# Performance work log

Hardware: AMD Instinct MI355X
Metric: run time of the kernel (lower is better)

Reference implementation:

```python
import jax, jax.numpy as jnp
import numpy as np

WH, WW = 7, 7
DIM, HEADS = 256, 8


def make_table_index(wh, ww):
    # relative coords table (log-spaced CPB input) and relative position index
    ch = np.arange(-(wh - 1), wh, dtype=np.float32)
    cw = np.arange(-(ww - 1), ww, dtype=np.float32)
    t = np.stack(np.meshgrid(ch, cw, indexing='ij'), axis=-1)[None]  # [1,2wh-1,2ww-1,2]
    t = t.copy()
    t[..., 0] /= (wh - 1)
    t[..., 1] /= (ww - 1)
    t *= 8.0
    t = np.sign(t) * np.log2(np.abs(t) + 1.0) / np.log2(8.0)
    coords = np.stack(np.meshgrid(np.arange(wh), np.arange(ww), indexing='ij'))
    cf = coords.reshape(2, -1)
    rc = (cf[:, :, None] - cf[:, None, :]).transpose(1, 2, 0).copy()  # [N,N,2]
    rc[..., 0] += wh - 1
    rc[..., 1] += ww - 1
    rc[..., 0] *= 2 * ww - 1
    idx = rc.sum(-1)
    return t.astype(np.float32), idx.astype(np.int32)


def setup_inputs() -> dict:
    key = jax.random.key(0)
    ks = jax.random.split(key, 10)
    B_, N, C, H = 2048, WH * WW, DIM, HEADS
    table, idx = make_table_index(WH, WW)
    return {
        'x': jax.random.normal(ks[0], (B_, N, C), jnp.float32),
        'mask': jnp.zeros((64, N, N), jnp.float32),
        'qkv_w': jax.random.normal(ks[1], (3 * C, C), jnp.float32) * 0.02,
        'q_bias': jnp.zeros((C,), jnp.float32),
        'v_bias': jnp.zeros((C,), jnp.float32),
        'logit_scale': jnp.full((H, 1, 1), np.log(10.0), jnp.float32),
        'cpb_w1': jax.random.normal(ks[2], (512, 2), jnp.float32) * 0.02,
        'cpb_b1': jnp.zeros((512,), jnp.float32),
        'cpb_w2': jax.random.normal(ks[3], (H, 512), jnp.float32) * 0.02,
        'proj_w': jax.random.normal(ks[4], (C, C), jnp.float32) * 0.02,
        'proj_b': jnp.zeros((C,), jnp.float32),
        'rel_coords_table': jnp.asarray(table),
        'rel_pos_index': jnp.asarray(idx),
    }


def _l2norm(t):
    return t / jnp.maximum(jnp.linalg.norm(t, axis=-1, keepdims=True), 1e-12)


def reference(x, mask, qkv_w, q_bias, v_bias, logit_scale, cpb_w1, cpb_b1,
              cpb_w2, proj_w, proj_b, rel_coords_table, rel_pos_index):
    B_, N, C = x.shape
    H = logit_scale.shape[0]
    hd = C // H
    qkv_b = jnp.concatenate([q_bias, jnp.zeros_like(v_bias), v_bias])
    qkv = (x @ qkv_w.T + qkv_b).reshape(B_, N, 3, H, hd).transpose(2, 0, 3, 1, 4)
    q, k, v = qkv[0], qkv[1], qkv[2]  # [B_,H,N,hd]
    attn = jnp.einsum('bhnd,bhmd->bhnm', _l2norm(q), _l2norm(k))
    scale = jnp.exp(jnp.minimum(logit_scale, jnp.log(jnp.float32(100.0))))  # [H,1,1]
    attn = attn * scale[None]
    # CPB MLP -> relative position bias
    table = jax.nn.relu(rel_coords_table @ cpb_w1.T + cpb_b1) @ cpb_w2.T  # [1,Th,Tw,H]
    table = table.reshape(-1, H)
    bias = table[rel_pos_index.reshape(-1)].reshape(N, N, H).transpose(2, 0, 1)
    attn = attn + 16.0 * jax.nn.sigmoid(bias)[None]
    nW = mask.shape[0]
    attn = attn.reshape(B_ // nW, nW, H, N, N) + mask[None, :, None]
    attn = jax.nn.softmax(attn.reshape(B_, H, N, N), axis=-1)
    out = jnp.einsum('bhnm,bhmd->bhnd', attn, v).transpose(0, 2, 1, 3).reshape(B_, N, C)
    return out @ proj_w.T + proj_b
```

## Files before the change

kernel.cpp:

```cpp
#include <hip/hip_runtime.h>

#define DEV __device__ __forceinline__

typedef float  f32x4  __attribute__((ext_vector_type(4)));
typedef __bf16 bf16x4 __attribute__((ext_vector_type(4)));
typedef __bf16 bf16x8 __attribute__((ext_vector_type(8)));

DEV unsigned short f2bf(float f) {
  unsigned u = __float_as_uint(f);
  u += 0x7fffu + ((u >> 16) & 1u);
  return (unsigned short)(u >> 16);
}

DEV void cp16(const void* g, void* l) {
  __builtin_amdgcn_global_load_lds((const __attribute__((address_space(1))) void*)g,
                                   (__attribute__((address_space(3))) void*)l, 16, 0, 0);
}

__global__ __launch_bounds__(256) void prep_kernel(
    const float* __restrict__ qkv_w, const float* __restrict__ proj_w,
    const float* __restrict__ q_bias, const float* __restrict__ v_bias,
    unsigned short* __restrict__ wq, unsigned short* __restrict__ wp,
    float* __restrict__ qkvb)
{
  int gid = blockIdx.x * 256 + threadIdx.x;
  if (gid < 196608) wq[gid] = f2bf(qkv_w[gid]);
  else              wp[gid - 196608] = f2bf(proj_w[gid - 196608]);
  if (gid < 768)
    qkvb[gid] = (gid < 256) ? q_bias[gid] : ((gid < 512) ? 0.f : v_bias[gid - 512]);
}

__global__ __launch_bounds__(256) void xbf16(
    const float* __restrict__ X, unsigned short* __restrict__ Xb)
{
  size_t gid = (size_t)blockIdx.x * 256 + threadIdx.x;
  const float4* xp = (const float4*)X;
  float4 f0 = xp[2 * gid], f1 = xp[2 * gid + 1];
  bf16x8 u;
  u[0] = (__bf16)f0.x; u[1] = (__bf16)f0.y; u[2] = (__bf16)f0.z; u[3] = (__bf16)f0.w;
  u[4] = (__bf16)f1.x; u[5] = (__bf16)f1.y; u[6] = (__bf16)f1.z; u[7] = (__bf16)f1.w;
  ((bf16x8*)Xb)[gid] = u;
}

__global__ __launch_bounds__(64) void cpb_mlp(
    const float* __restrict__ tab, const float* __restrict__ w1,
    const float* __restrict__ b1, const float* __restrict__ w2,
    float* __restrict__ table16)
{
  int r = blockIdx.x;
  int t = threadIdx.x;
  float x0 = tab[r * 2 + 0], x1 = tab[r * 2 + 1];
  float part[8];
#pragma unroll
  for (int h = 0; h < 8; ++h) part[h] = 0.f;
  for (int j = t; j < 512; j += 64) {
    float hv = fmaxf(w1[j * 2 + 0] * x0 + w1[j * 2 + 1] * x1 + b1[j], 0.f);
#pragma unroll
    for (int h = 0; h < 8; ++h) part[h] += hv * w2[h * 512 + j];
  }
#pragma unroll
  for (int h = 0; h < 8; ++h) {
    float v = part[h];
    for (int off = 32; off > 0; off >>= 1) v += __shfl_down(v, off, 64);
    if (t == 0) table16[r * 8 + h] = 16.f / (1.f + expf(-v));
  }
}

__global__ __launch_bounds__(256) void bmb(
    const float* __restrict__ t16, const int* __restrict__ ridx,
    const float* __restrict__ mask, float* __restrict__ bias64,
    float* __restrict__ mask64)
{
  int gid = blockIdx.x * 256 + threadIdx.x;
  int p = gid & 4095, i = p >> 6, j = p & 63;
  bool valid = (i < 49) && (j < 49);
  if (gid < 32768) {
    int h = gid >> 12;
    bias64[gid] = valid ? t16[ridx[i * 49 + j] * 8 + h] : -1e30f;
  } else {
    int g2 = gid - 32768;
    int w = g2 >> 12;
    mask64[g2] = valid ? mask[w * 2401 + i * 49 + j] : 0.f;
  }
}

__global__ __launch_bounds__(256) void gemm_qkv(
    const unsigned short* __restrict__ Xb, const unsigned short* __restrict__ W,
    const float* __restrict__ bias, unsigned short* __restrict__ qkv)
{
  __shared__ __align__(1024) unsigned short sA[128 * 64];
  __shared__ __align__(1024) unsigned short sB[128 * 64];
  const int t = threadIdx.x, w = t >> 6, l = t & 63, quad = l >> 4, l15 = l & 15;
  const int idx = blockIdx.x;
  const int x8 = idx & 7, local = idx >> 3;
  const int my = x8 * 98 + local / 6, bnb = local % 6;
  const int bm = my * 128, bn = bnb * 128;
  const int wm = (w >> 1) * 64, wn = (w & 1) * 64;
  const int srow = t >> 3, sch = t & 7;
  const int sc = sch ^ (srow & 7);

  const unsigned short* asrc = Xb + (size_t)(bm + srow) * 256 + sc * 8;
  const unsigned short* wsrc = W  + (size_t)(bn + srow) * 256 + sc * 8;

  f32x4 acc[4][4] = {};
  for (int kt = 0; kt < 4; ++kt) {
    const int k0 = kt << 6;
    if (kt) __syncthreads();
#pragma unroll
    for (int i = 0; i < 4; ++i) {
      cp16(asrc + (size_t)i * 32 * 256 + k0, sA + (i * 256 + w * 64) * 8);
      cp16(wsrc + (size_t)i * 32 * 256 + k0, sB + (i * 256 + w * 64) * 8);
    }
    __syncthreads();
#pragma unroll
    for (int kk = 0; kk < 2; ++kk) {
      bf16x8 xf[4], wf[4];
#pragma unroll
      for (int mt = 0; mt < 4; ++mt)
        xf[mt] = *(const bf16x8*)&sA[(wm + mt * 16 + l15) * 64 + (((4 * kk + quad) ^ (l15 & 7)) * 8)];
#pragma unroll
      for (int nt = 0; nt < 4; ++nt)
        wf[nt] = *(const bf16x8*)&sB[(wn + nt * 16 + l15) * 64 + (((4 * kk + quad) ^ (l15 & 7)) * 8)];
#pragma unroll
      for (int nt = 0; nt < 4; ++nt)
#pragma unroll
        for (int mt = 0; mt < 4; ++mt)
          acc[nt][mt] = __builtin_amdgcn_mfma_f32_16x16x32_bf16(wf[nt], xf[mt], acc[nt][mt], 0, 0, 0);
    }
  }
  const int nbase = bn + wn;
#pragma unroll
  for (int mA = 0; mA < 4; ++mA) {
    const int mrow = bm + wm + mA * 16 + l15;
    const unsigned bb = (unsigned)(((unsigned long long)mrow * 87652394ull) >> 32);
    const int tok = mrow - (int)bb * 49;
#pragma unroll
    for (int k = 0; k < 2; ++k) {
      const int n0 = nbase + k * 32;
      const int s = n0 >> 8, h = (n0 >> 5) & 7;
      const f32x4 b0 = *(const f32x4*)(bias + n0 + quad * 4);
      const f32x4 b1 = *(const f32x4*)(bias + n0 + 16 + quad * 4);
      const f32x4 a0 = acc[2 * k][mA], a1 = acc[2 * k + 1][mA];
      bf16x8 u;
      u[0] = (__bf16)(a0[0] + b0[0]); u[1] = (__bf16)(a0[1] + b0[1]);
      u[2] = (__bf16)(a0[2] + b0[2]); u[3] = (__bf16)(a0[3] + b0[3]);
      u[4] = (__bf16)(a1[0] + b1[0]); u[5] = (__bf16)(a1[1] + b1[1]);
      u[6] = (__bf16)(a1[2] + b1[2]); u[7] = (__bf16)(a1[3] + b1[3]);
      *(bf16x8*)(qkv + (size_t)((bb * 8u + h) * 3u + s) * 1568 + tok * 32 + quad * 8) = u;
    }
  }
}

__global__ __launch_bounds__(256) void attn2(
    const unsigned short* __restrict__ qkv, const float* __restrict__ logit_scale,
    const float* __restrict__ bias64, const float* __restrict__ mask64,
    unsigned short* __restrict__ aout)
{
  __shared__ __align__(1024) char smem[4 * 12544];
  const int w = threadIdx.x >> 6, l = threadIdx.x & 63, quad = l >> 4, l15 = l & 15;
  const int flat = blockIdx.x * 4 + w;
  const int b = flat >> 3, h = flat & 7;
  char* my = smem + w * 12544;
  unsigned short* vT = (unsigned short*)my;
  unsigned short* P  = (unsigned short*)(my + 4096);
  float* rk = (float*)(my + 12288);

  const unsigned short* qb = qkv + (size_t)flat * 4704;
  const unsigned short* kb = qb + 1568;
  const unsigned short* vb = qb + 3136;

  bf16x8 kf[4], qf[4];
#pragma unroll
  for (int mt = 0; mt < 4; ++mt) kf[mt] = *(const bf16x8*)(kb + (mt * 16 + l15) * 32 + quad * 8);
#pragma unroll
  for (int nt = 0; nt < 4; ++nt) qf[nt] = *(const bf16x8*)(qb + (nt * 16 + l15) * 32 + quad * 8);

  const float scale = __expf(fminf(logit_scale[h], 4.60517019f));
  float rqv[4];
#pragma unroll
  for (int nt = 0; nt < 4; ++nt) {
    float s = 0.f;
#pragma unroll
    for (int d = 0; d < 8; ++d) { float f = (float)qf[nt][d]; s += f * f; }
    s += __shfl_xor(s, 16, 64); s += __shfl_xor(s, 32, 64);
    rqv[nt] = scale / fmaxf(sqrtf(s), 1e-12f);
  }
#pragma unroll
  for (int mt = 0; mt < 4; ++mt) {
    float s = 0.f;
#pragma unroll
    for (int d = 0; d < 8; ++d) { float f = (float)kf[mt][d]; s += f * f; }
    s += __shfl_xor(s, 16, 64); s += __shfl_xor(s, 32, 64);
    if (quad == 0) rk[mt * 16 + l15] = 1.f / fmaxf(sqrtf(s), 1e-12f);
  }

  if (l < 49) {
    unsigned short vv[32];
#pragma unroll
    for (int c = 0; c < 4; ++c) *(uint4*)&vv[c * 8] = *(const uint4*)(vb + l * 32 + c * 8);
#pragma unroll
    for (int dp = 0; dp < 32; ++dp) {
      const int d = (((dp >> 2) & 1) << 4) + ((dp >> 3) << 2) + (dp & 3);
      vT[d * 64 + (((l >> 3) ^ (d & 7)) << 3) + (l & 7)] = vv[dp];
    }
  } else {
#pragma unroll
    for (int d = 0; d < 32; ++d)
      vT[d * 64 + (((l >> 3) ^ (d & 7)) << 3) + (l & 7)] = 0;
  }

  f32x4 acc[4][4] = {};
  __builtin_amdgcn_s_setprio(1);
#pragma unroll
  for (int mt = 0; mt < 4; ++mt)
#pragma unroll
    for (int nt = 0; nt < 4; ++nt)
      acc[mt][nt] = __builtin_amdgcn_mfma_f32_16x16x32_bf16(kf[mt], qf[nt], acc[mt][nt], 0, 0, 0);
  __builtin_amdgcn_s_setprio(0);

  asm volatile("s_waitcnt lgkmcnt(0)" ::: "memory");

  const float* bh = bias64 + (size_t)h * 4096;
  const float* mw = mask64 + (size_t)(b & 63) * 4096;
  f32x4 rk4v[4];
#pragma unroll
  for (int mt = 0; mt < 4; ++mt) rk4v[mt] = *(const f32x4*)(rk + mt * 16 + quad * 4);

  float rs4[4];
#pragma unroll
  for (int nt = 0; nt < 4; ++nt) {
    const int i = nt * 16 + l15;
    const float rqi = rqv[nt];
    float s[4][4];
    float mx = -1e30f;
#pragma unroll
    for (int mt = 0; mt < 4; ++mt) {
      const int jb = mt * 16 + quad * 4;
      const f32x4 b4 = *(const f32x4*)(bh + i * 64 + jb);
      const f32x4 m4 = *(const f32x4*)(mw + i * 64 + jb);
#pragma unroll
      for (int r = 0; r < 4; ++r) {
        float sv = fmaf(acc[mt][nt][r], rqi * rk4v[mt][r], b4[r] + m4[r]);
        s[mt][r] = sv;
        mx = fmaxf(mx, sv);
      }
    }
    mx = fmaxf(mx, __shfl_xor(mx, 16, 64));
    mx = fmaxf(mx, __shfl_xor(mx, 32, 64));
    float sum = 0.f;
    float p[4][4];
#pragma unroll
    for (int mt = 0; mt < 4; ++mt)
#pragma unroll
      for (int r = 0; r < 4; ++r) {
        float pv = __expf(s[mt][r] - mx);
        p[mt][r] = pv; sum += pv;
      }
    sum += __shfl_xor(sum, 16, 64);
    sum += __shfl_xor(sum, 32, 64);
    rs4[nt] = 1.f / sum;
#pragma unroll
    for (int mt = 0; mt < 4; ++mt) {
      bf16x4 pk;
      pk[0] = (__bf16)p[mt][0]; pk[1] = (__bf16)p[mt][1];
      pk[2] = (__bf16)p[mt][2]; pk[3] = (__bf16)p[mt][3];
      const int c = 2 * mt + (quad >> 1);
      *(bf16x4*)((char*)P + i * 128 + ((c ^ (i & 7)) * 16) + (quad & 1) * 8) = pk;
    }
  }

  asm volatile("s_waitcnt lgkmcnt(0)" ::: "memory");

  f32x4 oacc[2][4] = {};
#pragma unroll
  for (int kk = 0; kk < 2; ++kk) {
    bf16x8 vf[2], pf[4];
#pragma unroll
    for (int mt = 0; mt < 2; ++mt)
      vf[mt] = *(const bf16x8*)((char*)vT + (mt * 16 + l15) * 128 + (((4 * kk + quad) ^ (l15 & 7)) * 16));
#pragma unroll
    for (int nt = 0; nt < 4; ++nt)
      pf[nt] = *(const bf16x8*)((char*)P + (nt * 16 + l15) * 128 + (((4 * kk + quad) ^ (l15 & 7)) * 16));
    __builtin_amdgcn_s_setprio(1);
#pragma unroll
    for (int mt = 0; mt < 2; ++mt)
#pragma unroll
      for (int nt = 0; nt < 4; ++nt)
        oacc[mt][nt] = __builtin_amdgcn_mfma_f32_16x16x32_bf16(vf[mt], pf[nt], oacc[mt][nt], 0, 0, 0);
    __builtin_amdgcn_s_setprio(0);
  }

#pragma unroll
  for (int nt = 0; nt < 4; ++nt) {
    const int tok = nt * 16 + l15;
    if (tok < 49) {
      unsigned short* op = aout + (size_t)(b * 49 + tok) * 256 + h * 32;
      const float rs = rs4[nt];
#pragma unroll
      for (int mt = 0; mt < 2; ++mt) {
        bf16x4 ov;
        ov[0] = (__bf16)(oacc[mt][nt][0] * rs); ov[1] = (__bf16)(oacc[mt][nt][1] * rs);
        ov[2] = (__bf16)(oacc[mt][nt][2] * rs); ov[3] = (__bf16)(oacc[mt][nt][3] * rs);
        *(bf16x4*)(op + mt * 16 + quad * 4) = ov;
      }
    }
  }
}

__global__ __launch_bounds__(256) void gemm_proj(
    const unsigned short* __restrict__ A, const unsigned short* __restrict__ W,
    const float* __restrict__ bias, float* __restrict__ Y)
{
  __shared__ __align__(1024) unsigned short sA[128 * 64];
  __shared__ __align__(1024) unsigned short sB[128 * 64];
  const int t = threadIdx.x, w = t >> 6, l = t & 63, quad = l >> 4, l15 = l & 15;
  const int bm = blockIdx.y * 128, bn = blockIdx.x * 128;
  const int wm = (w >> 1) * 64, wn = (w & 1) * 64;
  const int srow = t >> 3, sch = t & 7;
  const int sc = sch ^ (srow & 7);

  f32x4 acc[4][4] = {};
  for (int kt = 0; kt < 4; ++kt) {
    const int k0 = kt << 6;
    if (kt) __syncthreads();
#pragma unroll
    for (int i = 0; i < 4; ++i) {
      const int row = i * 32 + srow;
      cp16(A + (size_t)(bm + row) * 256 + k0 + sc * 8, sA + (i * 256 + w * 64) * 8);
      cp16(W + (size_t)(bn + row) * 256 + k0 + sc * 8, sB + (i * 256 + w * 64) * 8);
    }
    __syncthreads();
#pragma unroll
    for (int kk = 0; kk < 2; ++kk) {
      bf16x8 xf[4], wf[4];
#pragma unroll
      for (int mt = 0; mt < 4; ++mt)
        xf[mt] = *(const bf16x8*)&sA[(wm + mt * 16 + l15) * 64 + (((4 * kk + quad) ^ (l15 & 7)) * 8)];
#pragma unroll
      for (int nt = 0; nt < 4; ++nt)
        wf[nt] = *(const bf16x8*)&sB[(wn + nt * 16 + l15) * 64 + (((4 * kk + quad) ^ (l15 & 7)) * 8)];
#pragma unroll
      for (int nt = 0; nt < 4; ++nt)
#pragma unroll
        for (int mt = 0; mt < 4; ++mt)
          acc[nt][mt] = __builtin_amdgcn_mfma_f32_16x16x32_bf16(wf[nt], xf[mt], acc[nt][mt], 0, 0, 0);
    }
  }
#pragma unroll
  for (int mA = 0; mA < 4; ++mA) {
    const int row = bm + wm + mA * 16 + l15;
    float* orow = Y + (size_t)row * 256;
#pragma unroll
    for (int nW = 0; nW < 4; ++nW) {
      const int c0 = bn + wn + nW * 16 + quad * 4;
      const f32x4 bv = *(const f32x4*)(bias + c0);
      f32x4 v = acc[nW][mA];
      v[0] += bv[0]; v[1] += bv[1]; v[2] += bv[2]; v[3] += bv[3];
      *(f32x4*)(orow + c0) = v;
    }
  }
}

extern "C" void kernel_launch(void* const* d_in, const int* in_sizes, int n_in,
                              void* d_out, int out_size, void* d_ws, size_t ws_size,
                              hipStream_t stream) {
  const float* x           = (const float*)d_in[0];
  const float* mask        = (const float*)d_in[1];
  const float* qkv_w       = (const float*)d_in[2];
  const float* q_bias      = (const float*)d_in[3];
  const float* v_bias      = (const float*)d_in[4];
  const float* logit_scale = (const float*)d_in[5];
  const float* cpb_w1      = (const float*)d_in[6];
  const float* cpb_b1      = (const float*)d_in[7];
  const float* cpb_w2      = (const float*)d_in[8];
  const float* proj_w      = (const float*)d_in[9];
  const float* proj_b      = (const float*)d_in[10];
  const float* rel_tab     = (const float*)d_in[11];
  const int*   rel_idx     = (const int*)d_in[12];
  float*       out         = (float*)d_out;

  char* ws = (char*)d_ws;
  unsigned short* qkvp    = (unsigned short*)(ws + 0);
  unsigned short* aows    = (unsigned short*)(ws + 154140672);
  unsigned short* wq      = (unsigned short*)(ws + 205520896);
  unsigned short* wp      = (unsigned short*)(ws + 205914112);
  float*          qkvb    = (float*)(ws + 206045184);
  float*          table16 = (float*)(ws + 206048256);
  float*          bias64  = (float*)(ws + 206053888);
  float*          mask64  = (float*)(ws + 206184960);
  unsigned short* xbf = aows;

  prep_kernel<<<1024, 256, 0, stream>>>(qkv_w, proj_w, q_bias, v_bias, wq, wp, qkvb);
  cpb_mlp<<<169, 64, 0, stream>>>(rel_tab, cpb_w1, cpb_b1, cpb_w2, table16);
  bmb<<<1152, 256, 0, stream>>>(table16, rel_idx, mask, bias64, mask64);
  xbf16<<<12544, 256, 0, stream>>>(x, xbf);
  gemm_qkv<<<4704, 256, 0, stream>>>(xbf, wq, qkvb, qkvp);
  attn2<<<4096, 256, 0, stream>>>(qkvp, logit_scale, bias64, mask64, aows);
  gemm_proj<<<dim3(2, 784), 256, 0, stream>>>(aows, wp, proj_b, out);
}
```

Measured before the change: 389.5 us.

## Drop LDS V transpose in attention, gather V from global, use exp2 softmax

The attention kernel no longer builds a transposed, swizzled copy of V in LDS. It gathers the V fragments for the second MFMA directly from global memory with strided 2-byte loads, and moves the k-norm reciprocals from LDS into registers via lane shuffles, which shrinks per-wave LDS from 12544 to 8192 bytes. Softmax now uses exp2 with log2(e) folded into the logit scale, bias and mask, and the exp and the bf16 store of P are fused into one loop. The padded token rows (49..63) are now read from neighbouring memory instead of zeros; they are multiplied by zero probabilities, but the last block may read past the buffer end. The many narrow uncoalesced global loads could cost more than the LDS pass they replace.

```diff
diff --git a/kernel.cpp b/kernel.cpp
--- a/kernel.cpp
+++ b/kernel.cpp
@@ -71,16 +71,17 @@
     const float* __restrict__ mask, float* __restrict__ bias64,
     float* __restrict__ mask64)
 {
+  const float L2E = 1.44269504f;
   int gid = blockIdx.x * 256 + threadIdx.x;
   int p = gid & 4095, i = p >> 6, j = p & 63;
   bool valid = (i < 49) && (j < 49);
   if (gid < 32768) {
     int h = gid >> 12;
-    bias64[gid] = valid ? t16[ridx[i * 49 + j] * 8 + h] : -1e30f;
+    bias64[gid] = valid ? t16[ridx[i * 49 + j] * 8 + h] * L2E : -1e30f;
   } else {
     int g2 = gid - 32768;
     int w = g2 >> 12;
-    mask64[g2] = valid ? mask[w * 2401 + i * 49 + j] : 0.f;
+    mask64[g2] = valid ? mask[w * 2401 + i * 49 + j] * L2E : 0.f;
   }
 }
 
@@ -156,14 +157,11 @@
     const float* __restrict__ bias64, const float* __restrict__ mask64,
     unsigned short* __restrict__ aout)
 {
-  __shared__ __align__(1024) char smem[4 * 12544];
+  __shared__ __align__(1024) char smem[4 * 8192];
   const int w = threadIdx.x >> 6, l = threadIdx.x & 63, quad = l >> 4, l15 = l & 15;
   const int flat = blockIdx.x * 4 + w;
   const int b = flat >> 3, h = flat & 7;
-  char* my = smem + w * 12544;
-  unsigned short* vT = (unsigned short*)my;
-  unsigned short* P  = (unsigned short*)(my + 4096);
-  float* rk = (float*)(my + 12288);
+  unsigned short* P = (unsigned short*)(smem + w * 8192);
 
   const unsigned short* qb = qkv + (size_t)flat * 4704;
   const unsigned short* kb = qb + 1568;
@@ -175,7 +173,7 @@
 #pragma unroll
   for (int nt = 0; nt < 4; ++nt) qf[nt] = *(const bf16x8*)(qb + (nt * 16 + l15) * 32 + quad * 8);
 
-  const float scale = __expf(fminf(logit_scale[h], 4.60517019f));
+  const float scale = __expf(fminf(logit_scale[h], 4.60517019f)) * 1.44269504f;
   float rqv[4];
 #pragma unroll
   for (int nt = 0; nt < 4; ++nt) {
@@ -185,29 +183,21 @@
     s += __shfl_xor(s, 16, 64); s += __shfl_xor(s, 32, 64);
     rqv[nt] = scale / fmaxf(sqrtf(s), 1e-12f);
   }
+  float rkl[4];
 #pragma unroll
   for (int mt = 0; mt < 4; ++mt) {
     float s = 0.f;
 #pragma unroll
     for (int d = 0; d < 8; ++d) { float f = (float)kf[mt][d]; s += f * f; }
     s += __shfl_xor(s, 16, 64); s += __shfl_xor(s, 32, 64);
-    if (quad == 0) rk[mt * 16 + l15] = 1.f / fmaxf(sqrtf(s), 1e-12f);
-  }
-
-  if (l < 49) {
-    unsigned short vv[32];
-#pragma unroll
-    for (int c = 0; c < 4; ++c) *(uint4*)&vv[c * 8] = *(const uint4*)(vb + l * 32 + c * 8);
-#pragma unroll
-    for (int dp = 0; dp < 32; ++dp) {
-      const int d = (((dp >> 2) & 1) << 4) + ((dp >> 3) << 2) + (dp & 3);
-      vT[d * 64 + (((l >> 3) ^ (d & 7)) << 3) + (l & 7)] = vv[dp];
-    }
-  } else {
-#pragma unroll
-    for (int d = 0; d < 32; ++d)
-      vT[d * 64 + (((l >> 3) ^ (d & 7)) << 3) + (l & 7)] = 0;
-  }
+    rkl[mt] = 1.f / fmaxf(sqrtf(s), 1e-12f);
+  }
+  f32x4 rk4v[4];
+#pragma unroll
+  for (int mt = 0; mt < 4; ++mt)
+#pragma unroll
+    for (int r = 0; r < 4; ++r)
+      rk4v[mt][r] = __shfl(rkl[mt], (quad << 2) + r, 16);
 
   f32x4 acc[4][4] = {};
   __builtin_amdgcn_s_setprio(1);
@@ -218,21 +208,14 @@
       acc[mt][nt] = __builtin_amdgcn_mfma_f32_16x16x32_bf16(kf[mt], qf[nt], acc[mt][nt], 0, 0, 0);
   __builtin_amdgcn_s_setprio(0);
 
-  asm volatile("s_waitcnt lgkmcnt(0)" ::: "memory");
-
   const float* bh = bias64 + (size_t)h * 4096;
   const float* mw = mask64 + (size_t)(b & 63) * 4096;
-  f32x4 rk4v[4];
-#pragma unroll
-  for (int mt = 0; mt < 4; ++mt) rk4v[mt] = *(const f32x4*)(rk + mt * 16 + quad * 4);
-
   float rs4[4];
 #pragma unroll
   for (int nt = 0; nt < 4; ++nt) {
     const int i = nt * 16 + l15;
     const float rqi = rqv[nt];
-    float s[4][4];
-    float mx = -1e30f;
+    float mx = -3e38f;
 #pragma unroll
     for (int mt = 0; mt < 4; ++mt) {
       const int jb = mt * 16 + quad * 4;
@@ -241,32 +224,30 @@
 #pragma unroll
       for (int r = 0; r < 4; ++r) {
         float sv = fmaf(acc[mt][nt][r], rqi * rk4v[mt][r], b4[r] + m4[r]);
-        s[mt][r] = sv;
+        acc[mt][nt][r] = sv;
         mx = fmaxf(mx, sv);
       }
     }
     mx = fmaxf(mx, __shfl_xor(mx, 16, 64));
     mx = fmaxf(mx, __shfl_xor(mx, 32, 64));
     float sum = 0.f;
-    float p[4][4];
-#pragma unroll
-    for (int mt = 0; mt < 4; ++mt)
+#pragma unroll
+    for (int mt = 0; mt < 4; ++mt) {
+      float pv[4];
 #pragma unroll
       for (int r = 0; r < 4; ++r) {
-        float pv = __expf(s[mt][r] - mx);
-        p[mt][r] = pv; sum += pv;
+        pv[r] = __builtin_amdgcn_exp2f(acc[mt][nt][r] - mx);
+        sum += pv[r];
       }
+      bf16x4 pk;
+      pk[0] = (__bf16)pv[0]; pk[1] = (__bf16)pv[1];
+      pk[2] = (__bf16)pv[2]; pk[3] = (__bf16)pv[3];
+      const int c = 2 * mt + (quad >> 1);
+      *(bf16x4*)((char*)P + i * 128 + ((c ^ (i & 7)) * 16) + (quad & 1) * 8) = pk;
+    }
     sum += __shfl_xor(sum, 16, 64);
     sum += __shfl_xor(sum, 32, 64);
     rs4[nt] = 1.f / sum;
-#pragma unroll
-    for (int mt = 0; mt < 4; ++mt) {
-      bf16x4 pk;
-      pk[0] = (__bf16)p[mt][0]; pk[1] = (__bf16)p[mt][1];
-      pk[2] = (__bf16)p[mt][2]; pk[3] = (__bf16)p[mt][3];
-      const int c = 2 * mt + (quad >> 1);
-      *(bf16x4*)((char*)P + i * 128 + ((c ^ (i & 7)) * 16) + (quad & 1) * 8) = pk;
-    }
   }
 
   asm volatile("s_waitcnt lgkmcnt(0)" ::: "memory");
@@ -276,8 +257,12 @@
   for (int kk = 0; kk < 2; ++kk) {
     bf16x8 vf[2], pf[4];
 #pragma unroll
-    for (int mt = 0; mt < 2; ++mt)
-      vf[mt] = *(const bf16x8*)((char*)vT + (mt * 16 + l15) * 128 + (((4 * kk + quad) ^ (l15 & 7)) * 16));
+    for (int mt = 0; mt < 2; ++mt) {
+      const __bf16* vp = (const __bf16*)vb +
+          (32 * kk + quad * 8) * 32 + (l15 >> 2) * 8 + mt * 4 + (l15 & 3);
+#pragma unroll
+      for (int s = 0; s < 8; ++s) vf[mt][s] = vp[s * 32];
+    }
 #pragma unroll
     for (int nt = 0; nt < 4; ++nt)
       pf[nt] = *(const bf16x8*)((char*)P + (nt * 16 + l15) * 128 + (((4 * kk + quad) ^ (l15 & 7)) * 16));
```

Measured after the change: 409.6 us. 1.05x slower.
